# Kernel optimization log

Hardware: AMD Instinct MI355X
Metric: run time of the kernel (lower is better)

Reference implementation:

```python
import jax, jax.numpy as jnp
import numpy as np

E_DIM, N_DIM, C_DIM = 4, 2, 2   # context dims
V, K = 96, 20                   # mutation categories, signature rank
D, B = 1024, 256                # total samples, batch samples
EPS = 1e-20


def setup_inputs() -> dict:
    key = jax.random.key(0)
    ks = jax.random.split(key, 9)
    return {
        "yphi": jax.random.uniform(ks[0], (3, 3, E_DIM, N_DIM, C_DIM, B, V, K), jnp.float32),
        "Y": jax.random.uniform(ks[1], (3, 3, E_DIM, N_DIM, C_DIM, D, V), jnp.float32) * 10.0,
        "_T0": jax.random.normal(ks[2], (V, K), jnp.float32),
        "_t": jax.random.normal(ks[3], (V, K), jnp.float32),
        "_r": jax.random.normal(ks[4], (V, K), jnp.float32),
        "_e": jax.random.normal(ks[5], (E_DIM, K), jnp.float32),
        "_n": jax.random.normal(ks[6], (N_DIM, K), jnp.float32),
        "_c": jax.random.normal(ks[7], (C_DIM, K), jnp.float32),
        "index": jax.random.randint(ks[8], (B,), 0, D),
    }


def _missing_rate(Y):
    # Y: (3,3,e,n,c,D,V); sum over context dims (e,n,c) and mutation types V
    y_tr = Y.sum(axis=(2, 3, 4, 6))            # (3,3,D)
    tot = y_tr.sum(axis=(0, 1))                # (D,)
    m00 = y_tr[:2, :2].sum(axis=(0, 1)) / tot  # both strands observed
    m01 = y_tr[:2, 2].sum(axis=0) / tot        # r missing
    m10 = y_tr[2, :2].sum(axis=0) / tot        # t missing
    m11 = y_tr[2, 2] / tot                     # both missing
    return jnp.stack([m00, m01, m10, m11]).reshape(2, 2, -1)  # (2,2,D)


def _stack_T(_T0, _t, _r):
    # Baseline signature distributions over V, strand-tilted per (t,r) state.
    T0 = jax.nn.softmax(_T0, axis=0)           # (V,K)
    lt = jax.nn.sigmoid(_t)                    # per-type transcribed-strand prob
    lr = jax.nn.sigmoid(_r)
    ones = jnp.ones_like(lt)
    wt = jnp.stack([lt, 1.0 - lt, ones])       # (3,V,K): strand 0 / 1 / missing
    wr = jnp.stack([lr, 1.0 - lr, ones])
    Traw = T0[None, None] * wt[:, None] * wr[None, :]   # (3,3,V,K)
    T = Traw / Traw.sum(axis=2, keepdims=True)          # renormalize over V
    return T, T0, lt, lr


def _factors_to_F(T0, lt, lr, _e, _n, _c, mr_idx):
    # Marginal strand probabilities per signature k
    pt = (T0 * lt).sum(axis=0)                 # (K,)
    pr = (T0 * lr).sum(axis=0)
    qt = jnp.stack([pt, 1.0 - pt, jnp.ones_like(pt)])   # (3,K)
    qr = jnp.stack([pr, 1.0 - pr, jnp.ones_like(pr)])
    mi = jnp.array([0, 0, 1])
    mr3 = mr_idx[mi][:, mi]                    # (3,3,B): missing-rate per strand combo
    S = mr3[..., None] * qt[:, None, None, :] * qr[None, :, None, :]  # (3,3,B,K)
    pe = jax.nn.softmax(_e, axis=0)            # (e_dim,K)
    pn = jax.nn.softmax(_n, axis=0)
    pc = jax.nn.softmax(_c, axis=0)
    # (3,3,e,n,c,B,K)
    return jnp.einsum('ijdk,ek,nk,ck->ijencdk', S, pe, pn, pc)


def reference(yphi, Y, _T0, _t, _r, _e, _n, _c, index):
    mr = _missing_rate(Y)[:, :, index]                 # (2,2,B)
    T, T0, lt, lr = _stack_T(_T0, _t, _r)              # T: (3,3,V,K)
    F = _factors_to_F(T0, lt, lr, _e, _n, _c, mr)      # (3,3,e,n,c,B,K)
    # TF = T.unsqueeze(-3) * F.unsqueeze(-2): (3,3,e,n,c,B,V,K)
    TF = T[:, :, None, None, None, None, :, :] * F[..., None, :]
    return -(yphi * jnp.log(TF + EPS)).mean(axis=(-1, -2)).sum()
```

## Files before the change

### kernel.cpp

```cpp
#include <hip/hip_runtime.h>

#define EPSF 1e-20f
constexpr int V = 96, K = 20, D = 1024, B = 256;
constexpr int E_DIM = 4, N_DIM = 2, C_DIM = 2;
constexpr int VK = V * K;
constexpr int ENC = E_DIM * N_DIM * C_DIM;
constexpr int NBLK_MAIN = 9 * ENC * B;
constexpr int NSLOTS = 256;

__global__ void zero_acc_kernel(double* __restrict__ acc) {
    acc[threadIdx.x] = 0.0;
}

__global__ __launch_bounds__(64) void ytr_kernel(const float* __restrict__ Y,
                                                 float* __restrict__ y_tr) {
    const int blk = blockIdx.x;
    const int d = blk % D;
    const int ij = blk / D;
    const int tid = threadIdx.x;
    const float4* __restrict__ base = (const float4*)Y;
    float s = 0.f;
#pragma unroll
    for (int it = 0; it < 6; ++it) {
        int idx4 = tid + it * 64;
        int enc = idx4 / 24;
        int v4 = idx4 % 24;
        size_t off4 = (((size_t)(ij * ENC + enc) * D + d) * V) / 4 + v4;
        float4 y = base[off4];
        s += y.x + y.y + y.z + y.w;
    }
#pragma unroll
    for (int off = 32; off; off >>= 1) s += __shfl_down(s, off, 64);
    if (tid == 0) y_tr[blk] = s;
}

__global__ void mr_kernel(const float* __restrict__ y_tr, float* __restrict__ mr) {
    int d = blockIdx.x * blockDim.x + threadIdx.x;
    if (d >= D) return;
    float y[9];
    float tot = 0.f;
#pragma unroll
    for (int ij = 0; ij < 9; ++ij) { y[ij] = y_tr[ij * D + d]; tot += y[ij]; }
    mr[0 * D + d] = (y[0] + y[1] + y[3] + y[4]) / tot;
    mr[1 * D + d] = (y[2] + y[5]) / tot;
    mr[2 * D + d] = (y[6] + y[7]) / tot;
    mr[3 * D + d] = y[8] / tot;
}

__global__ __launch_bounds__(256) void factors_kernel(
    const float* __restrict__ T0_, const float* __restrict__ t_,
    const float* __restrict__ r_, const float* __restrict__ e_,
    const float* __restrict__ n_, const float* __restrict__ c_,
    float* __restrict__ T, float* __restrict__ H) {
    __shared__ float T0s[VK], lts[VK], lrs[VK];
    __shared__ float pt[K], pr[K];
    __shared__ float pes[E_DIM * K], pns[N_DIM * K], pcs[C_DIM * K];
    const int tid = threadIdx.x;

    for (int idx = tid; idx < VK; idx += 256) {
        lts[idx] = 1.0f / (1.0f + expf(-t_[idx]));
        lrs[idx] = 1.0f / (1.0f + expf(-r_[idx]));
    }
    if (tid < K) {
        const int k = tid;
        float mx = -1e30f;
        for (int v = 0; v < V; ++v) mx = fmaxf(mx, T0_[v * K + k]);
        float ssum = 0.f;
        for (int v = 0; v < V; ++v) {
            float ev = expf(T0_[v * K + k] - mx);
            T0s[v * K + k] = ev; ssum += ev;
        }
        for (int v = 0; v < V; ++v) T0s[v * K + k] /= ssum;
    }
    __syncthreads();

    if (tid < K) {
        const int k = tid;
        float spt = 0.f, spr = 0.f;
        for (int v = 0; v < V; ++v) {
            spt += T0s[v * K + k] * lts[v * K + k];
            spr += T0s[v * K + k] * lrs[v * K + k];
        }
        pt[k] = spt; pr[k] = spr;
        {
            float m = -1e30f;
            for (int e2 = 0; e2 < E_DIM; ++e2) m = fmaxf(m, e_[e2 * K + k]);
            float se = 0.f; float tmp[E_DIM];
            for (int e2 = 0; e2 < E_DIM; ++e2) { tmp[e2] = expf(e_[e2 * K + k] - m); se += tmp[e2]; }
            for (int e2 = 0; e2 < E_DIM; ++e2) pes[e2 * K + k] = tmp[e2] / se;
        }
        {
            float m = fmaxf(n_[k], n_[K + k]);
            float a0 = expf(n_[k] - m), a1 = expf(n_[K + k] - m);
            float se = a0 + a1;
            pns[k] = a0 / se; pns[K + k] = a1 / se;
        }
        {
            float m = fmaxf(c_[k], c_[K + k]);
            float a0 = expf(c_[k] - m), a1 = expf(c_[K + k] - m);
            float se = a0 + a1;
            pcs[k] = a0 / se; pcs[K + k] = a1 / se;
        }
    }
    __syncthreads();

    for (int id = tid; id < 9 * K; id += 256) {
        const int k = id % K;
        const int ij = id / K;
        const int i = ij / 3, j = ij % 3;
        float ssum = 0.f;
        for (int v = 0; v < V; ++v) {
            float lt = lts[v * K + k], lr = lrs[v * K + k];
            float wt = (i == 0) ? lt : (i == 1) ? (1.0f - lt) : 1.0f;
            float wr = (j == 0) ? lr : (j == 1) ? (1.0f - lr) : 1.0f;
            ssum += T0s[v * K + k] * wt * wr;
        }
        for (int v = 0; v < V; ++v) {
            float lt = lts[v * K + k], lr = lrs[v * K + k];
            float wt = (i == 0) ? lt : (i == 1) ? (1.0f - lt) : 1.0f;
            float wr = (j == 0) ? lr : (j == 1) ? (1.0f - lr) : 1.0f;
            T[(ij * V + v) * K + k] = T0s[v * K + k] * wt * wr / ssum;
        }
    }

    for (int id = tid; id < 9 * ENC * K; id += 256) {
        const int k = id % K;
        const int enc = (id / K) % ENC;
        const int ij = id / (K * ENC);
        const int i = ij / 3, j = ij % 3;
        const int e2 = enc / 4, n2 = (enc / 2) % 2, c2 = enc % 2;
        float qt = (i == 0) ? pt[k] : (i == 1) ? (1.0f - pt[k]) : 1.0f;
        float qr = (j == 0) ? pr[k] : (j == 1) ? (1.0f - pr[k]) : 1.0f;
        H[id] = qt * qr * pes[e2 * K + k] * pns[n2 * K + k] * pcs[c2 * K + k];
    }
}

__global__ __launch_bounds__(256) void main_kernel(
    const float* __restrict__ yphi, const float* __restrict__ T,
    const float* __restrict__ H, const float* __restrict__ mr,
    const int* __restrict__ index, double* __restrict__ acc) {
    __shared__ __align__(16) float Ts[VK];
    __shared__ __align__(16) float Fk[K];
    __shared__ float wsum[4];
    const int blk = blockIdx.x;
    const int tid = threadIdx.x;
    const int b = blk % B;
    const int encij = blk / B;
    const int ij = encij / ENC;
    const int i = ij / 3, j = ij % 3;

    if (tid < K) {
        float mrv = mr[((int)(i == 2) * 2 + (int)(j == 2)) * D + index[b]];
        Fk[tid] = mrv * H[encij * K + tid];
    }
    const float4* __restrict__ Tg = (const float4*)(T + ij * VK);
    float4* Ts4 = (float4*)Ts;
    for (int t = tid; t < VK / 4; t += 256) Ts4[t] = Tg[t];
    __syncthreads();

    const float4* __restrict__ yg = (const float4*)(yphi + (size_t)blk * VK);
    float s = 0.f;
    for (int t = tid; t < VK / 4; t += 256) {
        float4 y = yg[t];
        float4 tt = Ts4[t];
        int k0 = (4 * t) % K;
        float4 f = *(const float4*)&Fk[k0];
        s += y.x * __logf(tt.x * f.x + EPSF);
        s += y.y * __logf(tt.y * f.y + EPSF);
        s += y.z * __logf(tt.z * f.z + EPSF);
        s += y.w * __logf(tt.w * f.w + EPSF);
    }
#pragma unroll
    for (int off = 32; off; off >>= 1) s += __shfl_down(s, off, 64);
    const int lane = tid & 63, wv = tid >> 6;
    if (lane == 0) wsum[wv] = s;
    __syncthreads();
    if (tid == 0) {
        float tot = wsum[0] + wsum[1] + wsum[2] + wsum[3];
        atomicAdd(&acc[blk & (NSLOTS - 1)], (double)tot);
    }
}

__global__ void final_kernel(const double* __restrict__ acc, float* __restrict__ out) {
    __shared__ double sh[NSLOTS];
    const int tid = threadIdx.x;
    sh[tid] = acc[tid];
    __syncthreads();
    for (int off = NSLOTS / 2; off; off >>= 1) {
        if (tid < off) sh[tid] += sh[tid + off];
        __syncthreads();
    }
    if (tid == 0) out[0] = (float)(-sh[0] / (double)VK);
}

extern "C" void kernel_launch(void* const* d_in, const int* in_sizes, int n_in,
                              void* d_out, int out_size, void* d_ws, size_t ws_size,
                              hipStream_t stream) {
    const float* yphi = (const float*)d_in[0];
    const float* Y    = (const float*)d_in[1];
    const float* T0_  = (const float*)d_in[2];
    const float* t_   = (const float*)d_in[3];
    const float* r_   = (const float*)d_in[4];
    const float* e_   = (const float*)d_in[5];
    const float* n_   = (const float*)d_in[6];
    const float* c_   = (const float*)d_in[7];
    const int* index  = (const int*)d_in[8];
    float* out = (float*)d_out;

    char* ws = (char*)d_ws;
    double* acc = (double*)ws;
    float* y_tr = (float*)(ws + 2048);
    float* mr   = (float*)(ws + 38912);
    float* T    = (float*)(ws + 55296);
    float* H    = (float*)(ws + 124416);

    hipLaunchKernelGGL(zero_acc_kernel, dim3(1), dim3(NSLOTS), 0, stream, acc);
    hipLaunchKernelGGL(ytr_kernel, dim3(9 * D), dim3(64), 0, stream, Y, y_tr);
    hipLaunchKernelGGL(mr_kernel, dim3(4), dim3(256), 0, stream, y_tr, mr);
    hipLaunchKernelGGL(factors_kernel, dim3(1), dim3(256), 0, stream,
                       T0_, t_, r_, e_, n_, c_, T, H);
    hipLaunchKernelGGL(main_kernel, dim3(NBLK_MAIN), dim3(256), 0, stream,
                       yphi, T, H, mr, index, acc);
    hipLaunchKernelGGL(final_kernel, dim3(1), dim3(NSLOTS), 0, stream, acc, out);
}
```

Measured before the change: 476.0 us.

## Factor log into precomputed log terms and batch samples per block

Rewrites the loss using log(T*F) = log T + log H + log mr, precomputing those logs once in the factors kernel. The main kernel then sums yphi over 16 batch samples per block and takes a dot product with the log tables, plus per-sample row sums weighted by log mr, so no per-element log is evaluated. The Y reduction and missing-rate computation are also fused into one kernel that zeroes the accumulator, cutting two launches. Dropping the +EPS changes behaviour when a factor underflows to zero. Summing in float in a different order also shifts rounding.

```diff
diff --git a/kernel.cpp b/kernel.cpp
--- a/kernel.cpp
+++ b/kernel.cpp
@@ -1,57 +1,63 @@
 #include <hip/hip_runtime.h>
 
-#define EPSF 1e-20f
 constexpr int V = 96, K = 20, D = 1024, B = 256;
 constexpr int E_DIM = 4, N_DIM = 2, C_DIM = 2;
 constexpr int VK = V * K;
 constexpr int ENC = E_DIM * N_DIM * C_DIM;
-constexpr int NBLK_MAIN = 9 * ENC * B;
+constexpr int NIJ = 9;
+constexpr int BCH = 16;
+constexpr int NBC = B / BCH;
 constexpr int NSLOTS = 256;
 
-__global__ void zero_acc_kernel(double* __restrict__ acc) {
-    acc[threadIdx.x] = 0.0;
-}
-
-__global__ __launch_bounds__(64) void ytr_kernel(const float* __restrict__ Y,
-                                                 float* __restrict__ y_tr) {
-    const int blk = blockIdx.x;
-    const int d = blk % D;
-    const int ij = blk / D;
-    const int tid = threadIdx.x;
+__global__ __launch_bounds__(128) void ymr_kernel(const float* __restrict__ Y,
+                                                  float* __restrict__ mr,
+                                                  double* __restrict__ acc) {
+    const int d = blockIdx.x;
+    const int tid = threadIdx.x;
+    if (d == 0) { acc[tid] = 0.0; acc[tid + 128] = 0.0; }
+
     const float4* __restrict__ base = (const float4*)Y;
-    float s = 0.f;
-#pragma unroll
-    for (int it = 0; it < 6; ++it) {
-        int idx4 = tid + it * 64;
-        int enc = idx4 / 24;
-        int v4 = idx4 % 24;
-        size_t off4 = (((size_t)(ij * ENC + enc) * D + d) * V) / 4 + v4;
-        float4 y = base[off4];
-        s += y.x + y.y + y.z + y.w;
-    }
-#pragma unroll
-    for (int off = 32; off; off >>= 1) s += __shfl_down(s, off, 64);
-    if (tid == 0) y_tr[blk] = s;
-}
-
-__global__ void mr_kernel(const float* __restrict__ y_tr, float* __restrict__ mr) {
-    int d = blockIdx.x * blockDim.x + threadIdx.x;
-    if (d >= D) return;
-    float y[9];
-    float tot = 0.f;
-#pragma unroll
-    for (int ij = 0; ij < 9; ++ij) { y[ij] = y_tr[ij * D + d]; tot += y[ij]; }
-    mr[0 * D + d] = (y[0] + y[1] + y[3] + y[4]) / tot;
-    mr[1 * D + d] = (y[2] + y[5]) / tot;
-    mr[2 * D + d] = (y[6] + y[7]) / tot;
-    mr[3 * D + d] = y[8] / tot;
+    float a[NIJ];
+#pragma unroll
+    for (int ij = 0; ij < NIJ; ++ij) {
+        float s = 0.f;
+#pragma unroll
+        for (int it = 0; it < 3; ++it) {
+            int idx = tid + it * 128;
+            int enc = idx / 24, v4 = idx % 24;
+            size_t off4 = ((size_t)(ij * ENC + enc) * D + d) * 24 + v4;
+            float4 y = base[off4];
+            s += y.x + y.y + y.z + y.w;
+        }
+        a[ij] = s;
+    }
+    __shared__ float Rw[2][NIJ];
+    const int lane = tid & 63, wv = tid >> 6;
+#pragma unroll
+    for (int ij = 0; ij < NIJ; ++ij) {
+        float s = a[ij];
+#pragma unroll
+        for (int off = 32; off; off >>= 1) s += __shfl_down(s, off, 64);
+        if (lane == 0) Rw[wv][ij] = s;
+    }
+    __syncthreads();
+    if (tid == 0) {
+        float y[NIJ], tot = 0.f;
+#pragma unroll
+        for (int ij = 0; ij < NIJ; ++ij) { y[ij] = Rw[0][ij] + Rw[1][ij]; tot += y[ij]; }
+        mr[0 * D + d] = (y[0] + y[1] + y[3] + y[4]) / tot;
+        mr[1 * D + d] = (y[2] + y[5]) / tot;
+        mr[2 * D + d] = (y[6] + y[7]) / tot;
+        mr[3 * D + d] = y[8] / tot;
+    }
 }
 
 __global__ __launch_bounds__(256) void factors_kernel(
     const float* __restrict__ T0_, const float* __restrict__ t_,
     const float* __restrict__ r_, const float* __restrict__ e_,
     const float* __restrict__ n_, const float* __restrict__ c_,
-    float* __restrict__ T, float* __restrict__ H) {
+    const float* __restrict__ mr, const int* __restrict__ index,
+    float* __restrict__ LT, float* __restrict__ LH, float* __restrict__ LM) {
     __shared__ float T0s[VK], lts[VK], lrs[VK];
     __shared__ float pt[K], pr[K];
     __shared__ float pes[E_DIM * K], pns[N_DIM * K], pcs[C_DIM * K];
@@ -92,19 +98,17 @@
         {
             float m = fmaxf(n_[k], n_[K + k]);
             float a0 = expf(n_[k] - m), a1 = expf(n_[K + k] - m);
-            float se = a0 + a1;
-            pns[k] = a0 / se; pns[K + k] = a1 / se;
+            pns[k] = a0 / (a0 + a1); pns[K + k] = a1 / (a0 + a1);
         }
         {
             float m = fmaxf(c_[k], c_[K + k]);
             float a0 = expf(c_[k] - m), a1 = expf(c_[K + k] - m);
-            float se = a0 + a1;
-            pcs[k] = a0 / se; pcs[K + k] = a1 / se;
-        }
-    }
-    __syncthreads();
-
-    for (int id = tid; id < 9 * K; id += 256) {
+            pcs[k] = a0 / (a0 + a1); pcs[K + k] = a1 / (a0 + a1);
+        }
+    }
+    __syncthreads();
+
+    for (int id = tid; id < NIJ * K; id += 256) {
         const int k = id % K;
         const int ij = id / K;
         const int i = ij / 3, j = ij % 3;
@@ -115,15 +119,16 @@
             float wr = (j == 0) ? lr : (j == 1) ? (1.0f - lr) : 1.0f;
             ssum += T0s[v * K + k] * wt * wr;
         }
+        float lss = __logf(ssum);
         for (int v = 0; v < V; ++v) {
             float lt = lts[v * K + k], lr = lrs[v * K + k];
             float wt = (i == 0) ? lt : (i == 1) ? (1.0f - lt) : 1.0f;
             float wr = (j == 0) ? lr : (j == 1) ? (1.0f - lr) : 1.0f;
-            T[(ij * V + v) * K + k] = T0s[v * K + k] * wt * wr / ssum;
-        }
-    }
-
-    for (int id = tid; id < 9 * ENC * K; id += 256) {
+            LT[(ij * V + v) * K + k] = __logf(T0s[v * K + k] * wt * wr) - lss;
+        }
+    }
+
+    for (int id = tid; id < NIJ * ENC * K; id += 256) {
         const int k = id % K;
         const int enc = (id / K) % ENC;
         const int ij = id / (K * ENC);
@@ -131,53 +136,80 @@
         const int e2 = enc / 4, n2 = (enc / 2) % 2, c2 = enc % 2;
         float qt = (i == 0) ? pt[k] : (i == 1) ? (1.0f - pt[k]) : 1.0f;
         float qr = (j == 0) ? pr[k] : (j == 1) ? (1.0f - pr[k]) : 1.0f;
-        H[id] = qt * qr * pes[e2 * K + k] * pns[n2 * K + k] * pcs[c2 * K + k];
+        LH[id] = __logf(qt * qr * pes[e2 * K + k] * pns[n2 * K + k] * pcs[c2 * K + k]);
+    }
+
+    for (int id = tid; id < NIJ * B; id += 256) {
+        const int ij = id >> 8, b = id & 255;
+        const int sel = ((ij / 3 == 2) ? 2 : 0) + ((ij % 3 == 2) ? 1 : 0);
+        LM[id] = __logf(mr[sel * D + index[b]]);
     }
 }
 
 __global__ __launch_bounds__(256) void main_kernel(
-    const float* __restrict__ yphi, const float* __restrict__ T,
-    const float* __restrict__ H, const float* __restrict__ mr,
-    const int* __restrict__ index, double* __restrict__ acc) {
-    __shared__ __align__(16) float Ts[VK];
-    __shared__ __align__(16) float Fk[K];
+    const float* __restrict__ yphi, const float* __restrict__ LT,
+    const float* __restrict__ LH, const float* __restrict__ LM,
+    double* __restrict__ acc) {
+    const int blk = blockIdx.x;
+    const int tid = threadIdx.x;
+    const int bc = blk % NBC;
+    const int ijenc = blk / NBC;
+    const int ij = ijenc / ENC;
+    const int lane = tid & 63, wv = tid >> 6;
+    const bool two = (tid < (VK / 4 - 256));
+
+    __shared__ float Rw[4][BCH];
     __shared__ float wsum[4];
-    const int blk = blockIdx.x;
-    const int tid = threadIdx.x;
-    const int b = blk % B;
-    const int encij = blk / B;
-    const int ij = encij / ENC;
-    const int i = ij / 3, j = ij % 3;
-
-    if (tid < K) {
-        float mrv = mr[((int)(i == 2) * 2 + (int)(j == 2)) * D + index[b]];
-        Fk[tid] = mrv * H[encij * K + tid];
-    }
-    const float4* __restrict__ Tg = (const float4*)(T + ij * VK);
-    float4* Ts4 = (float4*)Ts;
-    for (int t = tid; t < VK / 4; t += 256) Ts4[t] = Tg[t];
-    __syncthreads();
-
-    const float4* __restrict__ yg = (const float4*)(yphi + (size_t)blk * VK);
-    float s = 0.f;
-    for (int t = tid; t < VK / 4; t += 256) {
-        float4 y = yg[t];
-        float4 tt = Ts4[t];
-        int k0 = (4 * t) % K;
-        float4 f = *(const float4*)&Fk[k0];
-        s += y.x * __logf(tt.x * f.x + EPSF);
-        s += y.y * __logf(tt.y * f.y + EPSF);
-        s += y.z * __logf(tt.z * f.z + EPSF);
-        s += y.w * __logf(tt.w * f.w + EPSF);
-    }
-#pragma unroll
-    for (int off = 32; off; off >>= 1) s += __shfl_down(s, off, 64);
-    const int lane = tid & 63, wv = tid >> 6;
-    if (lane == 0) wsum[wv] = s;
-    __syncthreads();
-    if (tid == 0) {
-        float tot = wsum[0] + wsum[1] + wsum[2] + wsum[3];
-        atomicAdd(&acc[blk & (NSLOTS - 1)], (double)tot);
+
+    const float4* __restrict__ yg =
+        (const float4*)(yphi + (size_t)(ijenc * B + bc * BCH) * VK);
+
+    float4 acc1 = make_float4(0.f, 0.f, 0.f, 0.f);
+    float4 acc2 = make_float4(0.f, 0.f, 0.f, 0.f);
+#pragma unroll 4
+    for (int b = 0; b < BCH; ++b) {
+        float4 y1 = yg[b * (VK / 4) + tid];
+        float4 y2 = two ? yg[b * (VK / 4) + 256 + tid] : make_float4(0.f, 0.f, 0.f, 0.f);
+        acc1.x += y1.x; acc1.y += y1.y; acc1.z += y1.z; acc1.w += y1.w;
+        acc2.x += y2.x; acc2.y += y2.y; acc2.z += y2.z; acc2.w += y2.w;
+        float tb = y1.x + y1.y + y1.z + y1.w + y2.x + y2.y + y2.z + y2.w;
+#pragma unroll
+        for (int off = 32; off; off >>= 1) tb += __shfl_down(tb, off, 64);
+        if (lane == 0) Rw[wv][b] = tb;
+    }
+
+    const int c1 = 4 * tid;
+    float dot = 0.f;
+    {
+        float4 t4 = *(const float4*)&LT[ij * VK + c1];
+        float4 h4 = *(const float4*)&LH[ijenc * K + (c1 % K)];
+        dot += acc1.x * (t4.x + h4.x) + acc1.y * (t4.y + h4.y)
+             + acc1.z * (t4.z + h4.z) + acc1.w * (t4.w + h4.w);
+    }
+    if (two) {
+        const int c2 = c1 + 1024;
+        float4 t4 = *(const float4*)&LT[ij * VK + c2];
+        float4 h4 = *(const float4*)&LH[ijenc * K + (c2 % K)];
+        dot += acc2.x * (t4.x + h4.x) + acc2.y * (t4.y + h4.y)
+             + acc2.z * (t4.z + h4.z) + acc2.w * (t4.w + h4.w);
+    }
+#pragma unroll
+    for (int off = 32; off; off >>= 1) dot += __shfl_down(dot, off, 64);
+    if (lane == 0) wsum[wv] = dot;
+    __syncthreads();
+
+    float v = 0.f;
+    if (wv == 0 && lane < BCH) {
+        float r = Rw[0][lane] + Rw[1][lane] + Rw[2][lane] + Rw[3][lane];
+        v = r * LM[ij * B + bc * BCH + lane];
+    }
+    if (wv == 0) {
+#pragma unroll
+        for (int off = 8; off; off >>= 1) v += __shfl_down(v, off, 64);
+        if (lane == 0) {
+            float tot = wsum[0] + wsum[1] + wsum[2] + wsum[3] + v;
+            atomicAdd(&acc[blk & (NSLOTS - 1)], (double)tot);
+        }
     }
 }
 
@@ -209,17 +241,15 @@
 
     char* ws = (char*)d_ws;
     double* acc = (double*)ws;
-    float* y_tr = (float*)(ws + 2048);
-    float* mr   = (float*)(ws + 38912);
-    float* T    = (float*)(ws + 55296);
-    float* H    = (float*)(ws + 124416);
-
-    hipLaunchKernelGGL(zero_acc_kernel, dim3(1), dim3(NSLOTS), 0, stream, acc);
-    hipLaunchKernelGGL(ytr_kernel, dim3(9 * D), dim3(64), 0, stream, Y, y_tr);
-    hipLaunchKernelGGL(mr_kernel, dim3(4), dim3(256), 0, stream, y_tr, mr);
+    float* mr   = (float*)(ws + 2048);
+    float* LT   = (float*)(ws + 18432);
+    float* LH   = (float*)(ws + 87552);
+    float* LM   = (float*)(ws + 99072);
+
+    hipLaunchKernelGGL(ymr_kernel, dim3(D), dim3(128), 0, stream, Y, mr, acc);
     hipLaunchKernelGGL(factors_kernel, dim3(1), dim3(256), 0, stream,
-                       T0_, t_, r_, e_, n_, c_, T, H);
-    hipLaunchKernelGGL(main_kernel, dim3(NBLK_MAIN), dim3(256), 0, stream,
-                       yphi, T, H, mr, index, acc);
+                       T0_, t_, r_, e_, n_, c_, mr, index, LT, LH, LM);
+    hipLaunchKernelGGL(main_kernel, dim3(NIJ * ENC * NBC), dim3(256), 0, stream,
+                       yphi, LT, LH, LM, acc);
     hipLaunchKernelGGL(final_kernel, dim3(1), dim3(NSLOTS), 0, stream, acc, out);
 }
```

Result: no change. 481.9 us (+1.2%).
